# Kernel optimization log

Measured on AMD Instinct MI355X. Metric: run time of the kernel, lower is better.

The kernel has to match this reference:

```python
import jax, jax.numpy as jnp
import numpy as np

HEADS = 16
DIM_HEAD = 64
INNER = HEADS * DIM_HEAD  # 1024
QDIM = 1024
CDIM = 1024


def setup_inputs() -> dict:
    key = jax.random.key(0)
    ks = jax.random.split(key, 7)
    x = jax.random.normal(ks[0], (4, 2048, QDIM), dtype=jnp.float32)
    context = jax.random.normal(ks[1], (4, CDIM), dtype=jnp.float32)
    s = 0.02
    Wq = jax.random.normal(ks[2], (QDIM, INNER), dtype=jnp.float32) * s
    Wk = jax.random.normal(ks[3], (CDIM, INNER), dtype=jnp.float32) * s
    Wv = jax.random.normal(ks[4], (CDIM, INNER), dtype=jnp.float32) * s
    Wo = jax.random.normal(ks[5], (INNER, QDIM), dtype=jnp.float32) * s
    bo = jnp.zeros((QDIM,), dtype=jnp.float32)
    return {"x": x, "context": context, "Wq": Wq, "Wk": Wk, "Wv": Wv, "Wo": Wo, "bo": bo}


def reference(x, context, Wq, Wk, Wv, Wo, bo):
    B, N, _ = x.shape
    H, D = HEADS, DIM_HEAD
    scale = D ** (-0.5)
    # implicit cross attention: context (B, C) -> (B, 1, C)
    ctx = context[:, None, :]
    q = (x @ Wq).reshape(B, N, H, D).transpose(0, 2, 1, 3)      # (B,H,N,D)
    k = (ctx @ Wk).reshape(B, 1, H, D).transpose(0, 2, 1, 3)    # (B,H,1,D)
    v = (ctx @ Wv).reshape(B, 1, H, D).transpose(0, 2, 1, 3)
    # implicit cross-attn: prepend context token's k/v, append q as k/v
    k = jnp.concatenate([k, q], axis=2)  # (B,H,N+1,D)
    v = jnp.concatenate([v, q], axis=2)
    M = N + 1
    sim = jnp.einsum('bhid,bhjd->bhij', q, k) * scale  # (B,H,N,M)
    # causal mask with diagonal offset = k_len - q_len (implicit path)
    causal = jnp.tril(jnp.ones((N, M), dtype=bool), k=M - N)
    neg = -jnp.finfo(sim.dtype).max
    sim = jnp.where(causal[None, None], sim, neg)
    attn = jax.nn.softmax(sim, axis=-1)
    out = jnp.einsum('bhij,bhjd->bhid', attn, v)  # (B,H,N,D)
    out = out.transpose(0, 2, 1, 3).reshape(B, N, H * D)
    return out @ Wo + bo
```

## Files before the change

### kernel.cpp

```cpp
#include <hip/hip_runtime.h>
#include <stdint.h>

#define B_ 4
#define N_ 2048
#define H_ 16
#define D_ 64
#define QD 1024
#define SCALE 0.125f
#define LOG2E 1.44269504f
#define SC2 (SCALE * LOG2E)

typedef __bf16 bf16x8 __attribute__((ext_vector_type(8)));
typedef float f32x4 __attribute__((ext_vector_type(4)));
typedef float f32x16 __attribute__((ext_vector_type(16)));
typedef unsigned short u16x8 __attribute__((ext_vector_type(8)));
typedef unsigned short u16x4 __attribute__((ext_vector_type(4)));
typedef unsigned short ushort_t;

__device__ __forceinline__ unsigned short f2bf(float f) {
  union { float f; unsigned u; } x; x.f = f;
  unsigned r = (x.u + 0x7fffu + ((x.u >> 16) & 1u)) >> 16;
  return (unsigned short)r;
}

__device__ __forceinline__ void ldg2lds16(const void* g, void* l) {
  __builtin_amdgcn_global_load_lds(
      (const __attribute__((address_space(1))) void*)g,
      (__attribute__((address_space(3))) void*)l, 16, 0, 0);
}

__device__ __forceinline__ ushort_t bfbits(float f) {
  union { __bf16 b; ushort_t u; } x; x.b = (__bf16)f; return x.u;
}

__global__ __launch_bounds__(256) void k_cvt_bf16(const float* __restrict__ in,
                                                  ushort_t* __restrict__ out, int n8) {
  int i = blockIdx.x * 256 + threadIdx.x;
  if (i >= n8) return;
  const float4* p = (const float4*)in + (size_t)i * 2;
  float4 a = p[0], b = p[1];
  u16x8 r;
  r[0] = f2bf(a.x); r[1] = f2bf(a.y); r[2] = f2bf(a.z); r[3] = f2bf(a.w);
  r[4] = f2bf(b.x); r[5] = f2bf(b.y); r[6] = f2bf(b.z); r[7] = f2bf(b.w);
  *((u16x8*)out + i) = r;
}

__global__ __launch_bounds__(256) void k_transpose_w(const float* __restrict__ Wq,
    const float* __restrict__ Wo, ushort_t* __restrict__ WqT, ushort_t* __restrict__ WoT) {
  const float* W = blockIdx.z ? Wo : Wq;
  ushort_t* WT = blockIdx.z ? WoT : WqT;
  __shared__ float tile[64][65];
  int n0 = blockIdx.x * 64, k0 = blockIdx.y * 64;
  int tx = threadIdx.x & 63, ty = threadIdx.x >> 6;
#pragma unroll
  for (int i = 0; i < 64; i += 4)
    tile[ty + i][tx] = W[(size_t)(k0 + ty + i) * QD + n0 + tx];
  __syncthreads();
#pragma unroll
  for (int i = 0; i < 64; i += 4)
    WT[(size_t)(n0 + ty + i) * QD + k0 + tx] = f2bf(tile[tx][ty + i]);
}

__global__ __launch_bounds__(256) void k_ctx_partial(const float* __restrict__ ctx,
    const float* __restrict__ Wk, const float* __restrict__ Wv, float* __restrict__ part) {
  int ich = blockIdx.x;
  int ks = blockIdx.y;
  int kv = blockIdx.z;
  const float* W = kv ? Wv : Wk;
  __shared__ float cs[B_][128];
  int t = threadIdx.x;
  for (int i = t; i < B_ * 128; i += 256)
    cs[i >> 7][i & 127] = ctx[(size_t)(i >> 7) * QD + ks * 128 + (i & 127)];
  __syncthreads();
  int col = ich * 256 + t;
  float a0 = 0, a1 = 0, a2 = 0, a3 = 0;
  for (int k = 0; k < 128; k++) {
    float w = W[(size_t)(ks * 128 + k) * QD + col];
    a0 += cs[0][k] * w; a1 += cs[1][k] * w; a2 += cs[2][k] * w; a3 += cs[3][k] * w;
  }
  float* p = part + (size_t)(ks * 2 + kv) * (B_ * QD);
  p[0 * QD + col] = a0; p[1 * QD + col] = a1; p[2 * QD + col] = a2; p[3 * QD + col] = a3;
}

__global__ __launch_bounds__(256) void k_ctx_reduce(const float* __restrict__ part,
    float* __restrict__ kctx, float* __restrict__ vctx) {
  int idx = blockIdx.x * 256 + threadIdx.x;
  int kv = idx >> 12;
  int rest = idx & 4095;
  float acc = 0;
  for (int ks = 0; ks < 8; ks++) acc += part[(size_t)(ks * 2 + kv) * 4096 + rest];
  (kv ? vctx : kctx)[rest] = acc;
}

template <int BF16OUT, int WRITEQT>
__global__ __launch_bounds__(256) void k_gemm(const ushort_t* __restrict__ A,
    const ushort_t* __restrict__ Bm, ushort_t* __restrict__ Cb, float* __restrict__ Cf,
    const float* __restrict__ bias, ushort_t* __restrict__ qT) {
  __shared__ __align__(16) char arena[WRITEQT ? (128 * 136 * 2) : (128 * 32 * 2 * 2)];
  ushort_t* As = (ushort_t*)arena;
  ushort_t* Bs = (ushort_t*)arena + 128 * 32;
  const int wg = blockIdx.x;
  const int by = (wg & 7) * 8 + ((wg >> 3) & 7);
  const int bx = wg >> 6;
  const int t = threadIdx.x;
  const int w = t >> 6, l = t & 63;
  const int wr = w >> 1, wc = w & 1;
  const int lr = l & 15, lg = l >> 4;
  const int m0 = by * 128, n0 = bx * 128;
  f32x4 acc[4][4] = {};
  for (int k0 = 0; k0 < QD; k0 += 32) {
    ldg2lds16(&A[(size_t)(m0 + (t >> 2)) * QD + k0 + (t & 3) * 8], &As[t * 8]);
    ldg2lds16(&A[(size_t)(m0 + ((t + 256) >> 2)) * QD + k0 + (t & 3) * 8], &As[(t + 256) * 8]);
    ldg2lds16(&Bm[(size_t)(n0 + (t >> 2)) * QD + k0 + (t & 3) * 8], &Bs[t * 8]);
    ldg2lds16(&Bm[(size_t)(n0 + ((t + 256) >> 2)) * QD + k0 + (t & 3) * 8], &Bs[(t + 256) * 8]);
    __syncthreads();
    bf16x8 af[4], bfr[4];
#pragma unroll
    for (int m = 0; m < 4; m++)
      af[m] = *(const bf16x8*)&As[(wr * 64 + m * 16 + lr) * 32 + lg * 8];
#pragma unroll
    for (int n = 0; n < 4; n++)
      bfr[n] = *(const bf16x8*)&Bs[(wc * 64 + n * 16 + lr) * 32 + lg * 8];
#pragma unroll
    for (int m = 0; m < 4; m++)
#pragma unroll
      for (int n = 0; n < 4; n++)
        acc[m][n] = __builtin_amdgcn_mfma_f32_16x16x32_bf16(af[m], bfr[n], acc[m][n], 0, 0, 0);
    __syncthreads();
  }
#pragma unroll
  for (int m = 0; m < 4; m++) {
    int row = m0 + wr * 64 + m * 16 + lg * 4;
#pragma unroll
    for (int n = 0; n < 4; n++) {
      int col = n0 + wc * 64 + n * 16 + lr;
#pragma unroll
      for (int j = 0; j < 4; j++) {
        float v = acc[m][n][j];
        if constexpr (BF16OUT) {
          Cb[(size_t)(row + j) * QD + col] = f2bf(v);
        } else {
          Cf[(size_t)(row + j) * QD + col] = v + bias[col];
        }
      }
    }
  }
  if constexpr (WRITEQT) {
    ushort_t* T2 = (ushort_t*)arena;
#pragma unroll
    for (int m = 0; m < 4; m++) {
      int rowl = wr * 64 + m * 16 + lg * 4;
#pragma unroll
      for (int n = 0; n < 4; n++) {
        int col = wc * 64 + n * 16 + lr;
        u16x4 v;
#pragma unroll
        for (int j = 0; j < 4; j++) v[j] = f2bf(acc[m][n][j]);
        *(u16x4*)&T2[col * 136 + rowl] = v;
      }
    }
    __syncthreads();
    const int c = t & 127, r0 = (t >> 7) * 64;
    const int h = (n0 + c) >> 6, d = (n0 + c) & 63;
    const int b = m0 >> 11, nloc = (m0 & 2047) + r0;
    ushort_t* dst = qT + ((size_t)(b * 16 + h) * 64 + d) * (size_t)N_ + nloc;
#pragma unroll
    for (int i = 0; i < 8; i++)
      *(u16x8*)(dst + i * 8) = *(const u16x8*)&T2[c * 136 + r0 + i * 8];
  }
}

__global__ __launch_bounds__(256, 2) void k_attn10(
    const ushort_t* __restrict__ q, const ushort_t* __restrict__ qT,
    const float* __restrict__ kctx, const float* __restrict__ vctx,
    ushort_t* __restrict__ att) {
  const int wg = blockIdx.x;
  const int s = wg >> 6;
  const int bh = ((wg & 7) << 3) | ((wg >> 3) & 7);
  const int b = bh >> 4, h = bh & 15;
  const int t = threadIdx.x, w = t >> 6, l = t & 63;
  const int lq = l & 31, hi = l >> 5;

  __shared__ __align__(128) ushort_t Ks[2][2][4096];
  __shared__ __align__(128) ushort_t Vs[2][2][4096];

  const ushort_t* qbase = q + (size_t)b * N_ * QD + h * D_;
  const ushort_t* qtb = qT + (size_t)bh * D_ * N_;
  const float* kc = kctx + bh * D_;
  const float* vc = vctx + bh * D_;

  const int srow = t >> 3;
  const int scol = 8 * ((t & 7) ^ ((t >> 3) & 7));

#pragma unroll 1
  for (int pass = 0; pass < 2; ++pass) {
    const int qt = pass ? 15 - s : s;
    const int i0 = qt * 128;
    const int wq0 = i0 + w * 32;
    const int NI = qt + 1;

    __builtin_amdgcn_s_barrier();

    const ushort_t* stK = qbase + (size_t)srow * QD + scol;
    const ushort_t* stV = qtb + (size_t)srow * N_ + scol;

    auto stage = [&](int pr, int j) {
      ldg2lds16(stK, &Ks[pr][j][t * 8]);
      ldg2lds16(stK + (size_t)32 * QD, &Ks[pr][j][(t + 256) * 8]);
      ldg2lds16(stV, &Vs[pr][j][t * 8]);
      ldg2lds16(stV + (size_t)32 * N_, &Vs[pr][j][(t + 256) * 8]);
      stK += (size_t)64 * QD;
      stV += 64;
    };

    stage(0, 0);
    stage(0, 1);

    bf16x8 qf[4];
#pragma unroll
    for (int kk = 0; kk < 4; kk++)
      qf[kk] = *(const bf16x8*)&qbase[(size_t)(wq0 + lq) * QD + kk * 16 + hi * 8];

    float m2, lacc;
    f32x16 oacc[2];
    {
      float dot = 0.f;
#pragma unroll
      for (int kk = 0; kk < 4; kk++)
#pragma unroll
        for (int j = 0; j < 8; j++)
          dot += (float)qf[kk][j] * kc[kk * 16 + hi * 8 + j];
      dot += __shfl_xor(dot, 32);
      m2 = dot * SC2;
      lacc = 0.0f;
#pragma unroll
      for (int dt = 0; dt < 2; dt++)
#pragma unroll
        for (int r = 0; r < 16; r++)
          oacc[dt][r] = vc[dt * 32 + (r & 3) + 8 * (r >> 2) + 4 * hi];
    }

    auto body = [&](int tt, const char* ksb, const char* vsb) {
      const int j0 = tt * 64;
      if (j0 > wq0 + 31) return;

      f32x16 p[2];
      __builtin_amdgcn_s_setprio(1);
#pragma unroll
      for (int kb = 0; kb < 2; kb++) {
        f32x16 acc = {};
#pragma unroll
        for (int kk = 0; kk < 4; kk++) {
          bf16x8 kf = *(const bf16x8*)(ksb + (l & 31) * 128 + kb * 4096 +
                                       (((kk * 2 + hi) ^ (l & 7)) << 4));
          acc = __builtin_amdgcn_mfma_f32_32x32x16_bf16(kf, qf[kk], acc, 0, 0, 0);
        }
        p[kb] = acc;
      }
      __builtin_amdgcn_s_setprio(0);

      if (j0 + 63 > wq0) {
        const int qrel = wq0 - j0 + lq;
#pragma unroll
        for (int kb = 0; kb < 2; kb++)
#pragma unroll
          for (int r = 0; r < 16; r++) {
            int key = kb * 32 + (r & 3) + 8 * (r >> 2) + 4 * hi;
            if (key > qrel) p[kb][r] = -1e30f;
          }
      }

#pragma unroll
      for (int kb = 0; kb < 2; kb++)
#pragma unroll
        for (int r = 0; r < 16; r++)
          p[kb][r] = __builtin_exp2f(fmaf(p[kb][r], SC2, -m2));
      float s8[8];
#pragma unroll
      for (int r = 0; r < 8; r++)
        s8[r] = (p[0][r] + p[0][r + 8]) + (p[1][r] + p[1][r + 8]);
      float s4a = s8[0] + s8[4], s4b = s8[1] + s8[5];
      float s4c = s8[2] + s8[6], s4d = s8[3] + s8[7];
      lacc += (s4a + s4b) + (s4c + s4d);

#pragma unroll
      for (int kb = 0; kb < 2; kb++) {
        unsigned u[8];
#pragma unroll
        for (int i = 0; i < 8; i++) {
          float lo = p[kb][2 * i], hi2 = p[kb][2 * i + 1];
          asm("v_cvt_pk_bf16_f32 %0, %1, %2" : "=v"(u[i]) : "v"(lo), "v"(hi2));
        }
        asm("v_permlane32_swap_b32 %0, %1" : "+v"(u[0]), "+v"(u[2]));
        asm("v_permlane32_swap_b32 %0, %1" : "+v"(u[1]), "+v"(u[3]));
        asm("v_permlane32_swap_b32 %0, %1" : "+v"(u[4]), "+v"(u[6]));
        asm("v_permlane32_swap_b32 %0, %1" : "+v"(u[5]), "+v"(u[7]));
        union { unsigned u4[4]; bf16x8 v; } pf0, pf1;
        pf0.u4[0] = u[0]; pf0.u4[1] = u[1]; pf0.u4[2] = u[2]; pf0.u4[3] = u[3];
        pf1.u4[0] = u[4]; pf1.u4[1] = u[5]; pf1.u4[2] = u[6]; pf1.u4[3] = u[7];
        __builtin_amdgcn_s_setprio(1);
#pragma unroll
        for (int ks = 0; ks < 2; ks++) {
          const bf16x8 pf = ks ? pf1.v : pf0.v;
#pragma unroll
          for (int dt = 0; dt < 2; dt++) {
            bf16x8 vf = *(const bf16x8*)(vsb + (l & 31) * 128 + dt * 4096 +
                                         (((kb * 4 + ks * 2 + hi) ^ (l & 7)) << 4));
            oacc[dt] = __builtin_amdgcn_mfma_f32_32x32x16_bf16(vf, pf, oacc[dt], 0, 0, 0);
          }
        }
        __builtin_amdgcn_s_setprio(0);
      }
    };

    for (int it = 0; it < NI; ++it) {
      const int pr = it & 1;
      if (it + 1 < NI) {
        stage(pr ^ 1, 0);
        stage(pr ^ 1, 1);
        asm volatile("s_waitcnt vmcnt(8)" ::: "memory");
      } else {
        asm volatile("s_waitcnt vmcnt(0)" ::: "memory");
      }
      __builtin_amdgcn_s_barrier();

      body(2 * it,     (const char*)&Ks[pr][0][0], (const char*)&Vs[pr][0][0]);
      body(2 * it + 1, (const char*)&Ks[pr][1][0], (const char*)&Vs[pr][1][0]);
    }

    const float lsum = 1.0f + lacc + __shfl_xor(lacc, 32);
    const float inv = 1.0f / lsum;
    ushort_t* ob = att + (size_t)b * N_ * QD + (size_t)(wq0 + lq) * QD + h * D_;
#pragma unroll
    for (int dt = 0; dt < 2; dt++)
#pragma unroll
      for (int rq = 0; rq < 4; rq++) {
        union { ushort_t s4[4]; unsigned long long v; } o;
#pragma unroll
        for (int e = 0; e < 4; e++) o.s4[e] = bfbits(oacc[dt][rq * 4 + e] * inv);
        *(unsigned long long*)(ob + dt * 32 + 8 * rq + 4 * hi) = o.v;
      }
  }
}

extern "C" void kernel_launch(void* const* d_in, const int* in_sizes, int n_in,
                              void* d_out, int out_size, void* d_ws, size_t ws_size,
                              hipStream_t stream) {
  const float* x = (const float*)d_in[0];
  const float* ctx = (const float*)d_in[1];
  const float* Wq = (const float*)d_in[2];
  const float* Wk = (const float*)d_in[3];
  const float* Wv = (const float*)d_in[4];
  const float* Wo = (const float*)d_in[5];
  const float* bo = (const float*)d_in[6];
  float* out = (float*)d_out;

  char* ws = (char*)d_ws;
  size_t off = 0;
  ushort_t* xb = (ushort_t*)(ws + off);   off += (size_t)8192 * 1024 * 2;
  ushort_t* qb = (ushort_t*)(ws + off);   off += (size_t)8192 * 1024 * 2;
  ushort_t* attb = (ushort_t*)(ws + off); off += (size_t)8192 * 1024 * 2;
  ushort_t* WqT = (ushort_t*)(ws + off);  off += (size_t)1024 * 1024 * 2;
  ushort_t* WoT = (ushort_t*)(ws + off);  off += (size_t)1024 * 1024 * 2;
  float* kctx = (float*)(ws + off);       off += (size_t)4096 * 4;
  float* vctx = (float*)(ws + off);       off += (size_t)4096 * 4;
  float* part = (float*)(ws + off);       off += (size_t)16 * 4096 * 4;
  ushort_t* qT2 = (ushort_t*)(ws + off);  off += (size_t)8192 * 1024 * 2;

  k_cvt_bf16<<<dim3(4096), dim3(256), 0, stream>>>(x, xb, 8192 * 1024 / 8);
  k_transpose_w<<<dim3(16, 16, 2), dim3(256), 0, stream>>>(Wq, Wo, WqT, WoT);
  k_ctx_partial<<<dim3(4, 8, 2), dim3(256), 0, stream>>>(ctx, Wk, Wv, part);
  k_ctx_reduce<<<dim3(32), dim3(256), 0, stream>>>(part, kctx, vctx);
  k_gemm<1, 1><<<dim3(512), dim3(256), 0, stream>>>(xb, WqT, qb, nullptr, nullptr, qT2);
  k_attn10<<<dim3(512), dim3(256), 0, stream>>>(qb, qT2, kctx, vctx, attb);
  k_gemm<0, 0><<<dim3(512), dim3(256), 0, stream>>>(attb, WoT, nullptr, out, bo, nullptr);
}
```

Measured before the change: 149.1 us.

## Merge prep kernels into one launch and fold softmax scale into Q

The three preprocessing kernels (x conversion, weight transpose, context projection partials) are merged into one launch that dispatches on block index, removing two kernel launches and their gaps. In attention, the query fragment is pre-multiplied by scale*log2e, so the per-score fma before exp2 is dropped. The max subtraction is also removed and the context token weight becomes exp2(dot) rather than 1. This relies on scores staying small enough not to overflow exp2, and it adds an extra bf16 rounding of the scaled query, which the V side of the attention still uses unscaled from qT.

```diff
diff --git a/kernel.cpp b/kernel.cpp
--- a/kernel.cpp
+++ b/kernel.cpp
@@ -33,53 +33,54 @@
   union { __bf16 b; ushort_t u; } x; x.b = (__bf16)f; return x.u;
 }
 
-__global__ __launch_bounds__(256) void k_cvt_bf16(const float* __restrict__ in,
-                                                  ushort_t* __restrict__ out, int n8) {
-  int i = blockIdx.x * 256 + threadIdx.x;
-  if (i >= n8) return;
-  const float4* p = (const float4*)in + (size_t)i * 2;
-  float4 a = p[0], b = p[1];
-  u16x8 r;
-  r[0] = f2bf(a.x); r[1] = f2bf(a.y); r[2] = f2bf(a.z); r[3] = f2bf(a.w);
-  r[4] = f2bf(b.x); r[5] = f2bf(b.y); r[6] = f2bf(b.z); r[7] = f2bf(b.w);
-  *((u16x8*)out + i) = r;
-}
-
-__global__ __launch_bounds__(256) void k_transpose_w(const float* __restrict__ Wq,
-    const float* __restrict__ Wo, ushort_t* __restrict__ WqT, ushort_t* __restrict__ WoT) {
-  const float* W = blockIdx.z ? Wo : Wq;
-  ushort_t* WT = blockIdx.z ? WoT : WqT;
-  __shared__ float tile[64][65];
-  int n0 = blockIdx.x * 64, k0 = blockIdx.y * 64;
-  int tx = threadIdx.x & 63, ty = threadIdx.x >> 6;
-#pragma unroll
-  for (int i = 0; i < 64; i += 4)
-    tile[ty + i][tx] = W[(size_t)(k0 + ty + i) * QD + n0 + tx];
-  __syncthreads();
-#pragma unroll
-  for (int i = 0; i < 64; i += 4)
-    WT[(size_t)(n0 + ty + i) * QD + k0 + tx] = f2bf(tile[tx][ty + i]);
-}
-
-__global__ __launch_bounds__(256) void k_ctx_partial(const float* __restrict__ ctx,
-    const float* __restrict__ Wk, const float* __restrict__ Wv, float* __restrict__ part) {
-  int ich = blockIdx.x;
-  int ks = blockIdx.y;
-  int kv = blockIdx.z;
-  const float* W = kv ? Wv : Wk;
-  __shared__ float cs[B_][128];
-  int t = threadIdx.x;
-  for (int i = t; i < B_ * 128; i += 256)
-    cs[i >> 7][i & 127] = ctx[(size_t)(i >> 7) * QD + ks * 128 + (i & 127)];
-  __syncthreads();
-  int col = ich * 256 + t;
-  float a0 = 0, a1 = 0, a2 = 0, a3 = 0;
-  for (int k = 0; k < 128; k++) {
-    float w = W[(size_t)(ks * 128 + k) * QD + col];
-    a0 += cs[0][k] * w; a1 += cs[1][k] * w; a2 += cs[2][k] * w; a3 += cs[3][k] * w;
-  }
-  float* p = part + (size_t)(ks * 2 + kv) * (B_ * QD);
-  p[0 * QD + col] = a0; p[1 * QD + col] = a1; p[2 * QD + col] = a2; p[3 * QD + col] = a3;
+__global__ __launch_bounds__(256) void k_prep(const float* __restrict__ x,
+    ushort_t* __restrict__ xb, const float* __restrict__ Wq,
+    const float* __restrict__ Wo, ushort_t* __restrict__ WqT,
+    ushort_t* __restrict__ WoT, const float* __restrict__ ctx,
+    const float* __restrict__ Wk, const float* __restrict__ Wv,
+    float* __restrict__ part) {
+  __shared__ __align__(16) char arena[64 * 65 * 4];
+  const int wg = blockIdx.x;
+  const int t = threadIdx.x;
+  if (wg < 4096) {
+    int i = wg * 256 + t;
+    const float4* p = (const float4*)x + (size_t)i * 2;
+    float4 a = p[0], b = p[1];
+    u16x8 r;
+    r[0] = f2bf(a.x); r[1] = f2bf(a.y); r[2] = f2bf(a.z); r[3] = f2bf(a.w);
+    r[4] = f2bf(b.x); r[5] = f2bf(b.y); r[6] = f2bf(b.z); r[7] = f2bf(b.w);
+    *((u16x8*)xb + i) = r;
+  } else if (wg < 4608) {
+    const int wgl = wg - 4096;
+    const float* W = (wgl >> 8) ? Wo : Wq;
+    ushort_t* WT = (wgl >> 8) ? WoT : WqT;
+    float (*tile)[65] = (float(*)[65])arena;
+    int n0 = (wgl & 15) * 64, k0 = ((wgl >> 4) & 15) * 64;
+    int tx = t & 63, ty = t >> 6;
+#pragma unroll
+    for (int i = 0; i < 64; i += 4)
+      tile[ty + i][tx] = W[(size_t)(k0 + ty + i) * QD + n0 + tx];
+    __syncthreads();
+#pragma unroll
+    for (int i = 0; i < 64; i += 4)
+      WT[(size_t)(n0 + ty + i) * QD + k0 + tx] = f2bf(tile[tx][ty + i]);
+  } else {
+    const int wgl = wg - 4608;
+    const int ich = wgl & 3, ks = (wgl >> 2) & 7, kv = wgl >> 5;
+    const float* W = kv ? Wv : Wk;
+    float (*cs)[128] = (float(*)[128])arena;
+    for (int i = t; i < B_ * 128; i += 256)
+      cs[i >> 7][i & 127] = ctx[(size_t)(i >> 7) * QD + ks * 128 + (i & 127)];
+    __syncthreads();
+    int col = ich * 256 + t;
+    float a0 = 0, a1 = 0, a2 = 0, a3 = 0;
+    for (int k = 0; k < 128; k++) {
+      float w = W[(size_t)(ks * 128 + k) * QD + col];
+      a0 += cs[0][k] * w; a1 += cs[1][k] * w; a2 += cs[2][k] * w; a3 += cs[3][k] * w;
+    }
+    float* p = part + (size_t)(ks * 2 + kv) * (B_ * QD);
+    p[0 * QD + col] = a0; p[1 * QD + col] = a1; p[2 * QD + col] = a2; p[3 * QD + col] = a3;
+  }
 }
 
 __global__ __launch_bounds__(256) void k_ctx_reduce(const float* __restrict__ part,
@@ -170,7 +171,7 @@
   }
 }
 
-__global__ __launch_bounds__(256, 2) void k_attn10(
+__global__ __launch_bounds__(256, 2) void k_attn12(
     const ushort_t* __restrict__ q, const ushort_t* __restrict__ qT,
     const float* __restrict__ kctx, const float* __restrict__ vctx,
     ushort_t* __restrict__ att) {
@@ -218,10 +219,14 @@
 
     bf16x8 qf[4];
 #pragma unroll
-    for (int kk = 0; kk < 4; kk++)
+    for (int kk = 0; kk < 4; kk++) {
       qf[kk] = *(const bf16x8*)&qbase[(size_t)(wq0 + lq) * QD + kk * 16 + hi * 8];
-
-    float m2, lacc;
+#pragma unroll
+      for (int j = 0; j < 8; j++)
+        qf[kk][j] = (__bf16)((float)qf[kk][j] * SC2);
+    }
+
+    float ew, lacc;
     f32x16 oacc[2];
     {
       float dot = 0.f;
@@ -231,13 +236,13 @@
         for (int j = 0; j < 8; j++)
           dot += (float)qf[kk][j] * kc[kk * 16 + hi * 8 + j];
       dot += __shfl_xor(dot, 32);
-      m2 = dot * SC2;
+      ew = __builtin_exp2f(dot);
       lacc = 0.0f;
 #pragma unroll
       for (int dt = 0; dt < 2; dt++)
 #pragma unroll
         for (int r = 0; r < 16; r++)
-          oacc[dt][r] = vc[dt * 32 + (r & 3) + 8 * (r >> 2) + 4 * hi];
+          oacc[dt][r] = vc[dt * 32 + (r & 3) + 8 * (r >> 2) + 4 * hi] * ew;
     }
 
     auto body = [&](int tt, const char* ksb, const char* vsb) {
@@ -274,7 +279,7 @@
       for (int kb = 0; kb < 2; kb++)
 #pragma unroll
         for (int r = 0; r < 16; r++)
-          p[kb][r] = __builtin_exp2f(fmaf(p[kb][r], SC2, -m2));
+          p[kb][r] = __builtin_exp2f(p[kb][r]);
       float s8[8];
 #pragma unroll
       for (int r = 0; r < 8; r++)
@@ -328,7 +333,7 @@
       body(2 * it + 1, (const char*)&Ks[pr][1][0], (const char*)&Vs[pr][1][0]);
     }
 
-    const float lsum = 1.0f + lacc + __shfl_xor(lacc, 32);
+    const float lsum = ew + lacc + __shfl_xor(lacc, 32);
     const float inv = 1.0f / lsum;
     ushort_t* ob = att + (size_t)b * N_ * QD + (size_t)(wq0 + lq) * QD + h * D_;
 #pragma unroll
@@ -367,11 +372,10 @@
   float* part = (float*)(ws + off);       off += (size_t)16 * 4096 * 4;
   ushort_t* qT2 = (ushort_t*)(ws + off);  off += (size_t)8192 * 1024 * 2;
 
-  k_cvt_bf16<<<dim3(4096), dim3(256), 0, stream>>>(x, xb, 8192 * 1024 / 8);
-  k_transpose_w<<<dim3(16, 16, 2), dim3(256), 0, stream>>>(Wq, Wo, WqT, WoT);
-  k_ctx_partial<<<dim3(4, 8, 2), dim3(256), 0, stream>>>(ctx, Wk, Wv, part);
+  k_prep<<<dim3(4672), dim3(256), 0, stream>>>(x, xb, Wq, Wo, WqT, WoT,
+                                               ctx, Wk, Wv, part);
   k_ctx_reduce<<<dim3(32), dim3(256), 0, stream>>>(part, kctx, vctx);
   k_gemm<1, 1><<<dim3(512), dim3(256), 0, stream>>>(xb, WqT, qb, nullptr, nullptr, qT2);
-  k_attn10<<<dim3(512), dim3(256), 0, stream>>>(qb, qT2, kctx, vctx, attb);
+  k_attn12<<<dim3(512), dim3(256), 0, stream>>>(qb, qT2, kctx, vctx, attb);
   k_gemm<0, 0><<<dim3(512), dim3(256), 0, stream>>>(attb, WoT, nullptr, out, bo, nullptr);
 }
```

New measurement: 143.5 us. 3.7% less time.
